# Performance work log

Measured on AMD Instinct MI355X. Metric: run time of the kernel, lower is better.

Reference implementation:

```python
import jax, jax.numpy as jnp
import numpy as np

DN = ('NCHW', 'OIHW', 'NCHW')  # dimension numbers for all convs


def _dwconv(x, w, dim):
    # depthwise conv, valid padding; w: (dim,1,kh,kw)
    return jax.lax.conv_general_dilated(
        x, w, window_strides=(1, 1), padding='VALID',
        dimension_numbers=DN, feature_group_count=dim)


def setup_inputs() -> dict:
    key = jax.random.key(0)
    ks = jax.random.split(key, 5)
    B, C, H, W = 16, 256, 96, 96
    REP_K = 3
    x = jax.random.normal(ks[0], (B, C, H, W), dtype=jnp.float32)
    meta_pe = jax.random.normal(ks[1], (1, C, H, 1), dtype=jnp.float32) * 0.02
    weight = jax.random.normal(ks[2], (C, 1, H, 1), dtype=jnp.float32) * 0.02
    bias = jnp.zeros((C,), dtype=jnp.float32)
    rep_weight = jax.random.normal(ks[3], (C, 1, REP_K, 1), dtype=jnp.float32) * 0.02
    return {'x': x, 'meta_pe': meta_pe, 'weight': weight, 'bias': bias,
            'rep_weight': rep_weight}


def reference(x, meta_pe, weight, bias, rep_weight):
    # type == 'H': circular padding / conv along the H axis (kernels (K,1))
    dim = x.shape[1]
    rep_k = rep_weight.shape[2]
    # positional embedding add (broadcast over batch and W)
    x = x + meta_pe
    # local branch: circular pad by rep_k-1 rows, small depthwise conv
    x_cat = jnp.concatenate([x, x[:, :, :rep_k - 1, :]], axis=2)
    x_rep = _dwconv(x_cat, rep_weight, dim)
    # global branch: circular pad by H-1 rows, full-height depthwise conv + bias
    x_cat = jnp.concatenate([x, x[:, :, :-1, :]], axis=2)
    x_gcc = _dwconv(x_cat, weight, dim) + bias[None, :, None, None]
    return x_rep + x_gcc
```

## Files before the change

kernel.cpp:

```cpp
#include <hip/hip_runtime.h>

#define B_    16
#define C_    256
#define HH    96
#define WW    96
#define W4    24
#define TYN   8
#define HPT   12
#define TPB   (W4 * TYN)

__global__ __launch_bounds__(TPB, 3) void fused_circ_conv(
    const float* __restrict__ x,
    const float* __restrict__ meta_pe,
    const float* __restrict__ weight,
    const float* __restrict__ bias,
    const float* __restrict__ rep_weight,
    float* __restrict__ out)
{
    __shared__ float sX[HH * WW];
    __shared__ float sWext[2 * HH];

    const int tid = threadIdx.x;
    const int blk = blockIdx.x;
    const int c = blk & (C_ - 1);

    const size_t base = (size_t)blk * (HH * WW);
    const float4* __restrict__ xg4 = (const float4*)(x + base);

    {
        int k = (tid < HH) ? tid : (tid - HH);
        float wv = weight[c * HH + k];
        if (k < 3) wv += rep_weight[c * 3 + k];
        sWext[tid] = wv;
    }

    {
        float4* sX4 = (float4*)sX;
        const float* mp = meta_pe + c * HH;
#pragma unroll
        for (int r = 0; r < 12; ++r) {
            int i = tid + TPB * r;
            float4 v = xg4[i];
            float m = mp[i / W4];
            v.x += m; v.y += m; v.z += m; v.w += m;
            sX4[i] = v;
        }
    }
    __syncthreads();

    const int tx = tid % W4;
    const int ty = tid / W4;
    const int h0 = ty * HPT;

    float4 acc[HPT];
#pragma unroll
    for (int i = 0; i < HPT; ++i) acc[i] = make_float4(0.f, 0.f, 0.f, 0.f);

    float win[12];
#pragma unroll
    for (int t = 1; t < 12; ++t) win[t] = sWext[84 + t - h0];

    const float4* __restrict__ xrow = (const float4*)sX + tx;
    const float* __restrict__ wrow = sWext + (96 - h0);

    for (int jj = 0; jj < 96; jj += 12) {
#pragma unroll
        for (int r = 0; r < 12; ++r) {
            const int j = jj + r;
            win[r] = wrow[j];
            float4 xv = xrow[j * W4];
#pragma unroll
            for (int i = 0; i < HPT; ++i) {
                float wv = win[(r - i + 12) % 12];
                acc[i].x += wv * xv.x;
                acc[i].y += wv * xv.y;
                acc[i].z += wv * xv.z;
                acc[i].w += wv * xv.w;
            }
        }
    }

    const float bv = bias[c];
    float4* og4 = (float4*)(out + base);
#pragma unroll
    for (int i = 0; i < HPT; ++i) {
        float4 v = acc[i];
        v.x += bv; v.y += bv; v.z += bv; v.w += bv;
        og4[(h0 + i) * W4 + tx] = v;
    }
}

extern "C" void kernel_launch(void* const* d_in, const int* in_sizes, int n_in,
                              void* d_out, int out_size, void* d_ws, size_t ws_size,
                              hipStream_t stream) {
    const float* x          = (const float*)d_in[0];
    const float* meta_pe    = (const float*)d_in[1];
    const float* weight     = (const float*)d_in[2];
    const float* bias       = (const float*)d_in[3];
    const float* rep_weight = (const float*)d_in[4];
    float* out = (float*)d_out;

    fused_circ_conv<<<dim3(B_ * C_), dim3(TPB), 0, stream>>>(
        x, meta_pe, weight, bias, rep_weight, out);
}
```

Baseline: 274.3 us.

## Double-buffer LDS row loads and vectorize weight window loads in conv loop

Restructures the inner convolution loop so that the next six input rows are read from shared memory into a second register buffer while FMAs run on the current buffer. The weight window is now loaded as float4 and shifted in registers instead of one scalar shared-memory load per row. The meta_pe index is computed directly as ty+8r, dropping an integer division. This should hide LDS latency and cut shared-memory instructions, at the cost of more registers (two x buffers plus the weight window), which could limit occupancy.

```diff
diff --git a/kernel.cpp b/kernel.cpp
--- a/kernel.cpp
+++ b/kernel.cpp
@@ -9,6 +9,24 @@
 #define HPT   12
 #define TPB   (W4 * TYN)
 
+#define WGET(e) ( ((e)&3)==0 ? ww[(e)>>2].x \
+                : ((e)&3)==1 ? ww[(e)>>2].y \
+                : ((e)&3)==2 ? ww[(e)>>2].z \
+                :              ww[(e)>>2].w )
+
+#define FMA_HALF(RBASE, XBUF)                                     \
+    _Pragma("unroll")                                             \
+    for (int r = 0; r < 6; ++r) {                                 \
+        _Pragma("unroll")                                         \
+        for (int i = 0; i < HPT; ++i) {                           \
+            const float wv = WGET(12 + (RBASE) + r - i);          \
+            acc[i].x += wv * XBUF[r].x;                           \
+            acc[i].y += wv * XBUF[r].y;                           \
+            acc[i].z += wv * XBUF[r].z;                           \
+            acc[i].w += wv * XBUF[r].w;                           \
+        }                                                         \
+    }
+
 __global__ __launch_bounds__(TPB, 3) void fused_circ_conv(
     const float* __restrict__ x,
     const float* __restrict__ meta_pe,
@@ -17,8 +35,8 @@
     const float* __restrict__ rep_weight,
     float* __restrict__ out)
 {
-    __shared__ float sX[HH * WW];
-    __shared__ float sWext[2 * HH];
+    __shared__ __align__(16) float sX[HH * WW];
+    __shared__ __align__(16) float sWext[2 * HH];
 
     const int tid = threadIdx.x;
     const int blk = blockIdx.x;
@@ -26,6 +44,10 @@
 
     const size_t base = (size_t)blk * (HH * WW);
     const float4* __restrict__ xg4 = (const float4*)(x + base);
+
+    const int tx = tid % W4;
+    const int ty = tid / W4;
+    const int h0 = ty * HPT;
 
     {
         int k = (tid < HH) ? tid : (tid - HH);
@@ -41,44 +63,49 @@
         for (int r = 0; r < 12; ++r) {
             int i = tid + TPB * r;
             float4 v = xg4[i];
-            float m = mp[i / W4];
+            float m = mp[ty + 8 * r];
             v.x += m; v.y += m; v.z += m; v.w += m;
             sX4[i] = v;
         }
     }
     __syncthreads();
 
-    const int tx = tid % W4;
-    const int ty = tid / W4;
-    const int h0 = ty * HPT;
-
     float4 acc[HPT];
 #pragma unroll
     for (int i = 0; i < HPT; ++i) acc[i] = make_float4(0.f, 0.f, 0.f, 0.f);
 
-    float win[12];
+    const float4* __restrict__ xq = (const float4*)sX + tx;
+    const float4* __restrict__ w4 = (const float4*)(sWext + (84 - h0));
+
+    float4 ww[6], wnxt[3], xA[6], xB[6];
+
 #pragma unroll
-    for (int t = 1; t < 12; ++t) win[t] = sWext[84 + t - h0];
+    for (int q = 0; q < 6; ++q) ww[q] = w4[q];
+#pragma unroll
+    for (int t = 0; t < 6; ++t) xA[t] = xq[t * W4];
 
-    const float4* __restrict__ xrow = (const float4*)sX + tx;
-    const float* __restrict__ wrow = sWext + (96 - h0);
+#pragma unroll 1
+    for (int g = 0; g < 7; ++g) {
+#pragma unroll
+        for (int t = 0; t < 6; ++t) xB[t] = xq[(g * 12 + 6 + t) * W4];
+#pragma unroll
+        for (int q = 0; q < 3; ++q) wnxt[q] = w4[3 * g + 6 + q];
 
-    for (int jj = 0; jj < 96; jj += 12) {
+        FMA_HALF(0, xA)
+
 #pragma unroll
-        for (int r = 0; r < 12; ++r) {
-            const int j = jj + r;
-            win[r] = wrow[j];
-            float4 xv = xrow[j * W4];
+        for (int t = 0; t < 6; ++t) xA[t] = xq[(g * 12 + 12 + t) * W4];
+
+        FMA_HALF(6, xB)
+
 #pragma unroll
-            for (int i = 0; i < HPT; ++i) {
-                float wv = win[(r - i + 12) % 12];
-                acc[i].x += wv * xv.x;
-                acc[i].y += wv * xv.y;
-                acc[i].z += wv * xv.z;
-                acc[i].w += wv * xv.w;
-            }
-        }
+        for (int q = 0; q < 3; ++q) { ww[q] = ww[q + 3]; ww[q + 3] = wnxt[q]; }
     }
+
+#pragma unroll
+    for (int t = 0; t < 6; ++t) xB[t] = xq[(90 + t) * W4];
+    FMA_HALF(0, xA)
+    FMA_HALF(6, xB)
 
     const float bv = bias[c];
     float4* og4 = (float4*)(out + base);
```

Result: no change. 274.6 us (+0.1%).

## Split each channel plane into width strips and load weights as float4 windows

Applied to the files above, without the earlier changes.

Each (batch, channel) plane is now split into three width strips of 32 columns, each handled by its own block. This triples the grid and cuts shared memory per block to about 12 KB, so more blocks can be resident (launch bounds raised to 6). Each thread now computes 4 output rows instead of 12. Weights are read from shared memory as float4 groups of 16 per 12-row step instead of using a rolling scalar window. The trade-off is that every block reloads the extended weight vector, and each thread gets less register reuse of the x values it reads from shared memory.

```diff
diff --git a/kernel.cpp b/kernel.cpp
--- a/kernel.cpp
+++ b/kernel.cpp
@@ -4,12 +4,19 @@
 #define C_    256
 #define HH    96
 #define WW    96
-#define W4    24
-#define TYN   8
-#define HPT   12
-#define TPB   (W4 * TYN)
+#define WQ    24
+#define TW4   8
+#define NS    3
+#define TYN   24
+#define HPT   4
+#define TPB   (TW4 * TYN)
 
-__global__ __launch_bounds__(TPB, 3) void fused_circ_conv(
+#define WGET(e) ( ((e)&3)==0 ? wq[(e)>>2].x \
+                : ((e)&3)==1 ? wq[(e)>>2].y \
+                : ((e)&3)==2 ? wq[(e)>>2].z \
+                :              wq[(e)>>2].w )
+
+__global__ __launch_bounds__(TPB, 6) void fused_circ_conv(
     const float* __restrict__ x,
     const float* __restrict__ meta_pe,
     const float* __restrict__ weight,
@@ -17,61 +24,60 @@
     const float* __restrict__ rep_weight,
     float* __restrict__ out)
 {
-    __shared__ float sX[HH * WW];
-    __shared__ float sWext[2 * HH];
+    __shared__ __align__(16) float sX[HH * TW4 * 4];
+    __shared__ __align__(16) float sWx[2 * HH];
 
     const int tid = threadIdx.x;
     const int blk = blockIdx.x;
-    const int c = blk & (C_ - 1);
+    const int bc  = blk / NS;
+    const int s   = blk - bc * NS;
+    const int c   = bc & (C_ - 1);
 
-    const size_t base = (size_t)blk * (HH * WW);
-    const float4* __restrict__ xg4 = (const float4*)(x + base);
+    const int tx = tid % TW4;
+    const int ty = tid / TW4;
+    const int h0 = ty * HPT;
+
+    const size_t base = (size_t)bc * (HH * WW);
+    const float4* __restrict__ xg4 = (const float4*)(x + base) + TW4 * s;
 
     {
         int k = (tid < HH) ? tid : (tid - HH);
         float wv = weight[c * HH + k];
         if (k < 3) wv += rep_weight[c * 3 + k];
-        sWext[tid] = wv;
+        sWx[tid] = wv;
     }
 
     {
         float4* sX4 = (float4*)sX;
         const float* mp = meta_pe + c * HH;
 #pragma unroll
-        for (int r = 0; r < 12; ++r) {
-            int i = tid + TPB * r;
-            float4 v = xg4[i];
-            float m = mp[i / W4];
+        for (int r = 0; r < 4; ++r) {
+            float4 v = xg4[(ty + TYN * r) * WQ + tx];
+            float m = mp[ty + TYN * r];
             v.x += m; v.y += m; v.z += m; v.w += m;
-            sX4[i] = v;
+            sX4[tid + TPB * r] = v;
         }
     }
     __syncthreads();
-
-    const int tx = tid % W4;
-    const int ty = tid / W4;
-    const int h0 = ty * HPT;
 
     float4 acc[HPT];
 #pragma unroll
     for (int i = 0; i < HPT; ++i) acc[i] = make_float4(0.f, 0.f, 0.f, 0.f);
 
-    float win[12];
+    const float4* __restrict__ xq = (const float4*)sX + tx;
+    const float4* __restrict__ wqb = (const float4*)sWx + (23 - ty);
+
+#pragma unroll 1
+    for (int g = 0; g < 8; ++g) {
+        float4 wq[4];
 #pragma unroll
-    for (int t = 1; t < 12; ++t) win[t] = sWext[84 + t - h0];
-
-    const float4* __restrict__ xrow = (const float4*)sX + tx;
-    const float* __restrict__ wrow = sWext + (96 - h0);
-
-    for (int jj = 0; jj < 96; jj += 12) {
+        for (int q = 0; q < 4; ++q) wq[q] = wqb[3 * g + q];
 #pragma unroll
         for (int r = 0; r < 12; ++r) {
-            const int j = jj + r;
-            win[r] = wrow[j];
-            float4 xv = xrow[j * W4];
+            float4 xv = xq[(12 * g + r) * TW4];
 #pragma unroll
             for (int i = 0; i < HPT; ++i) {
-                float wv = win[(r - i + 12) % 12];
+                const float wv = WGET(4 + r - i);
                 acc[i].x += wv * xv.x;
                 acc[i].y += wv * xv.y;
                 acc[i].z += wv * xv.z;
@@ -81,12 +87,12 @@
     }
 
     const float bv = bias[c];
-    float4* og4 = (float4*)(out + base);
+    float4* og4 = (float4*)(out + base) + TW4 * s;
 #pragma unroll
     for (int i = 0; i < HPT; ++i) {
         float4 v = acc[i];
         v.x += bv; v.y += bv; v.z += bv; v.w += bv;
-        og4[(h0 + i) * W4 + tx] = v;
+        og4[(h0 + i) * WQ + tx] = v;
     }
 }
 
@@ -100,6 +106,6 @@
     const float* rep_weight = (const float*)d_in[4];
     float* out = (float*)d_out;
 
-    fused_circ_conv<<<dim3(B_ * C_), dim3(TPB), 0, stream>>>(
+    fused_circ_conv<<<dim3(B_ * C_ * NS), dim3(TPB), 0, stream>>>(
         x, meta_pe, weight, bias, rep_weight, out);
 }
```

After: 267.6 us. 2.4% less time.

## Compute circulant depthwise conv with fp16 split-precision MFMA instead of FP32 FMAs

Applied to the files above, without the earlier changes.

Recasts each per-channel 96x96 circular convolution as a circulant-matrix times input-matrix product and computes it with 32x32x16 fp16 MFMA instructions. Each wave handles 32 columns and three 32-row output tiles. FP32 accuracy is approximated by splitting both operands into high and low fp16 parts and issuing three MFMAs per k-step. The input now goes straight from global memory into registers instead of being staged in shared memory, which removes the large LDS buffer and lets occupancy rise to 4 blocks per SM. The trade-offs are reduced precision, since the lo*lo term is dropped, and strided, less coalesced global loads and stores.

```diff
diff --git a/kernel.cpp b/kernel.cpp
--- a/kernel.cpp
+++ b/kernel.cpp
@@ -1,15 +1,15 @@
 #include <hip/hip_runtime.h>
 
-#define B_    16
-#define C_    256
-#define HH    96
-#define WW    96
-#define W4    24
-#define TYN   8
-#define HPT   12
-#define TPB   (W4 * TYN)
+#define B_   16
+#define C_   256
+#define HH   96
+#define WW   96
+#define TPB  192
 
-__global__ __launch_bounds__(TPB, 3) void fused_circ_conv(
+typedef _Float16 half8 __attribute__((ext_vector_type(8)));
+typedef float   f32x16 __attribute__((ext_vector_type(16)));
+
+__global__ __launch_bounds__(TPB, 4) void fused_circ_conv_mfma(
     const float* __restrict__ x,
     const float* __restrict__ meta_pe,
     const float* __restrict__ weight,
@@ -17,76 +17,78 @@
     const float* __restrict__ rep_weight,
     float* __restrict__ out)
 {
-    __shared__ float sX[HH * WW];
-    __shared__ float sWext[2 * HH];
+    __shared__ float sW[2 * HH];
+    __shared__ float sPE[HH];
 
     const int tid = threadIdx.x;
     const int blk = blockIdx.x;
-    const int c = blk & (C_ - 1);
-
+    const int c   = blk & (C_ - 1);
     const size_t base = (size_t)blk * (HH * WW);
-    const float4* __restrict__ xg4 = (const float4*)(x + base);
 
     {
         int k = (tid < HH) ? tid : (tid - HH);
         float wv = weight[c * HH + k];
         if (k < 3) wv += rep_weight[c * 3 + k];
-        sWext[tid] = wv;
-    }
-
-    {
-        float4* sX4 = (float4*)sX;
-        const float* mp = meta_pe + c * HH;
-#pragma unroll
-        for (int r = 0; r < 12; ++r) {
-            int i = tid + TPB * r;
-            float4 v = xg4[i];
-            float m = mp[i / W4];
-            v.x += m; v.y += m; v.z += m; v.w += m;
-            sX4[i] = v;
-        }
+        sW[tid] = wv;
+        if (tid < HH) sPE[tid] = meta_pe[c * HH + tid];
     }
     __syncthreads();
 
-    const int tx = tid % W4;
-    const int ty = tid / W4;
-    const int h0 = ty * HPT;
+    const int lane = tid & 63;
+    const int wvid = tid >> 6;
+    const int r32  = lane & 31;
+    const int g    = lane >> 5;
 
-    float4 acc[HPT];
+    const float* __restrict__ xcol = x + base + (wvid * 32 + r32);
+    float bx[48];
 #pragma unroll
-    for (int i = 0; i < HPT; ++i) acc[i] = make_float4(0.f, 0.f, 0.f, 0.f);
+    for (int kt = 0; kt < 6; ++kt)
+#pragma unroll
+        for (int e = 0; e < 8; ++e)
+            bx[kt * 8 + e] = xcol[(kt * 16 + g * 8 + e) * WW];
 
-    float win[12];
+    half8 bh[6], bl[6];
 #pragma unroll
-    for (int t = 1; t < 12; ++t) win[t] = sWext[84 + t - h0];
-
-    const float4* __restrict__ xrow = (const float4*)sX + tx;
-    const float* __restrict__ wrow = sWext + (96 - h0);
-
-    for (int jj = 0; jj < 96; jj += 12) {
+    for (int kt = 0; kt < 6; ++kt) {
 #pragma unroll
-        for (int r = 0; r < 12; ++r) {
-            const int j = jj + r;
-            win[r] = wrow[j];
-            float4 xv = xrow[j * W4];
-#pragma unroll
-            for (int i = 0; i < HPT; ++i) {
-                float wv = win[(r - i + 12) % 12];
-                acc[i].x += wv * xv.x;
-                acc[i].y += wv * xv.y;
-                acc[i].z += wv * xv.z;
-                acc[i].w += wv * xv.w;
-            }
+        for (int e = 0; e < 8; ++e) {
+            float v = bx[kt * 8 + e] + sPE[kt * 16 + g * 8 + e];
+            _Float16 h = (_Float16)v;
+            bh[kt][e] = h;
+            bl[kt][e] = (_Float16)(v - (float)h);
         }
     }
 
     const float bv = bias[c];
-    float4* og4 = (float4*)(out + base);
+
+#pragma unroll 1
+    for (int m = 0; m < 3; ++m) {
+        f32x16 acc;
 #pragma unroll
-    for (int i = 0; i < HPT; ++i) {
-        float4 v = acc[i];
-        v.x += bv; v.y += bv; v.z += bv; v.w += bv;
-        og4[(h0 + i) * W4 + tx] = v;
+        for (int i = 0; i < 16; ++i) acc[i] = 0.f;
+
+#pragma unroll
+        for (int kt = 0; kt < 6; ++kt) {
+            const float* wp = sW + (96 + kt * 16 + g * 8 - m * 32 - r32);
+            half8 ah, al;
+#pragma unroll
+            for (int e = 0; e < 8; ++e) {
+                float w_ = wp[e];
+                _Float16 h = (_Float16)w_;
+                ah[e] = h;
+                al[e] = (_Float16)(w_ - (float)h);
+            }
+            acc = __builtin_amdgcn_mfma_f32_32x32x16_f16(ah, bh[kt], acc, 0, 0, 0);
+            acc = __builtin_amdgcn_mfma_f32_32x32x16_f16(al, bh[kt], acc, 0, 0, 0);
+            acc = __builtin_amdgcn_mfma_f32_32x32x16_f16(ah, bl[kt], acc, 0, 0, 0);
+        }
+
+        float* __restrict__ op = out + base + (wvid * 32 + r32);
+#pragma unroll
+        for (int reg = 0; reg < 16; ++reg) {
+            int row = m * 32 + (reg & 3) + 8 * (reg >> 2) + 4 * g;
+            op[row * WW] = acc[reg] + bv;
+        }
     }
 }
 
@@ -100,6 +102,6 @@
     const float* rep_weight = (const float*)d_in[4];
     float* out = (float*)d_out;
 
-    fused_circ_conv<<<dim3(B_ * C_), dim3(TPB), 0, stream>>>(
+    fused_circ_conv_mfma<<<dim3(B_ * C_), dim3(TPB), 0, stream>>>(
         x, meta_pe, weight, bias, rep_weight, out);
 }
```

After: 267.1 us. 1.03x faster.
